# Optimization experiments

Hardware: AMD Instinct MI355X
Metric: run time of the kernel (lower is better)

Reference implementation:

```python
import jax, jax.numpy as jnp
import numpy as np

NEG_SLOPE = 0.1

def lrelu(x):
    return jnp.where(x >= 0, x, NEG_SLOPE * x)

def conv2d(x, w, b, padding=0, dilation=1):
    y = jax.lax.conv_general_dilated(
        x, w, window_strides=(1, 1),
        padding=[(padding, padding), (padding, padding)],
        rhs_dilation=(dilation, dilation),
        dimension_numbers=('NCHW', 'OIHW', 'NCHW'))
    return y + b[None, :, None, None]

def res_aspp(x, p):
    r1 = lrelu(conv2d(x, p['a1_w'], p['a1_b'], padding=1, dilation=1))
    r2 = lrelu(conv2d(x, p['a2_w'], p['a2_b'], padding=2, dilation=2))
    r3 = lrelu(conv2d(x, p['a3_w'], p['a3_b'], padding=4, dilation=4))
    r = conv2d(jnp.concatenate((r1, r2, r3), axis=1), p['ar_w'], p['ar_b'])
    return x + r

def deform_conv2d(x, offset, w, b):
    # x: [B,C,H,W], offset: [B,2*K,H,W] torchvision layout (y,x) per 3x3 tap
    B, C, H, W = x.shape
    KH = KW = 3
    K = KH * KW
    pad = 1
    off = offset.reshape(B, K, 2, H, W)
    ky, kx = jnp.meshgrid(jnp.arange(KH), jnp.arange(KW), indexing='ij')
    ky = ky.reshape(K).astype(x.dtype)
    kx = kx.reshape(K).astype(x.dtype)
    hh = jnp.arange(H, dtype=x.dtype)
    ww = jnp.arange(W, dtype=x.dtype)
    # sampling positions [B,K,H,W]
    py = off[:, :, 0] + (hh[None, None, :, None] - pad + ky[None, :, None, None])
    px = off[:, :, 1] + (ww[None, None, None, :] - pad + kx[None, :, None, None])
    y0 = jnp.floor(py)
    x0 = jnp.floor(px)
    wy = (py - y0)[:, None]  # [B,1,K,H,W]
    wx = (px - x0)[:, None]
    y0i = y0.astype(jnp.int32)
    x0i = x0.astype(jnp.int32)
    x_flat = x.reshape(B, C, H * W)

    def gather(iy, ix):
        valid = ((iy >= 0) & (iy < H) & (ix >= 0) & (ix < W)).astype(x.dtype)
        idx = jnp.clip(iy, 0, H - 1) * W + jnp.clip(ix, 0, W - 1)  # [B,K,H,W]
        v = jax.vmap(lambda xb, ib: xb[:, ib])(x_flat, idx.reshape(B, -1))
        return v.reshape(B, C, K, H, W) * valid[:, None]

    samp = (gather(y0i, x0i) * (1 - wy) * (1 - wx)
            + gather(y0i, x0i + 1) * (1 - wy) * wx
            + gather(y0i + 1, x0i) * wy * (1 - wx)
            + gather(y0i + 1, x0i + 1) * wy * wx)
    out = jnp.einsum('bckhw,ock->bohw', samp, w.reshape(w.shape[0], C, K))
    return out + b[None, :, None, None]

def setup_inputs() -> dict:
    key = jax.random.key(0)
    ks = jax.random.split(key, 16)
    B, C, H, W = 4, 64, 160, 160
    Cout = 64
    s = 0.05
    d = {
        'in_aux': jax.random.normal(ks[0], (B, C, H, W), jnp.float32),
        'in_ref': jax.random.normal(ks[1], (B, C, H, W), jnp.float32),
        'w01': jax.random.normal(ks[2], (Cout, 2 * C, 1, 1), jnp.float32) * s,
        'b01': jnp.zeros((Cout,), jnp.float32),
        'a1_w': jax.random.normal(ks[3], (Cout, Cout, 3, 3), jnp.float32) * s,
        'a1_b': jnp.zeros((Cout,), jnp.float32),
        'a2_w': jax.random.normal(ks[4], (Cout, Cout, 3, 3), jnp.float32) * s,
        'a2_b': jnp.zeros((Cout,), jnp.float32),
        'a3_w': jax.random.normal(ks[5], (Cout, Cout, 3, 3), jnp.float32) * s,
        'a3_b': jnp.zeros((Cout,), jnp.float32),
        'ar_w': jax.random.normal(ks[6], (Cout, 3 * Cout, 1, 1), jnp.float32) * s,
        'ar_b': jnp.zeros((Cout,), jnp.float32),
        'w02': jax.random.normal(ks[7], (18, Cout, 1, 1), jnp.float32) * s,
        'b02': jnp.zeros((18,), jnp.float32),
        'dw': jax.random.normal(ks[8], (Cout, C, 3, 3), jnp.float32) * s,
        'db': jnp.zeros((Cout,), jnp.float32),
    }
    return d

def reference(in_aux, in_ref, w01, b01, a1_w, a1_b, a2_w, a2_b, a3_w, a3_b,
              ar_w, ar_b, w02, b02, dw, db):
    cat_x = jnp.concatenate((in_aux, in_ref), axis=1)
    off_x = lrelu(conv2d(cat_x, w01, b01))
    p = {'a1_w': a1_w, 'a1_b': a1_b, 'a2_w': a2_w, 'a2_b': a2_b,
         'a3_w': a3_w, 'a3_b': a3_b, 'ar_w': ar_w, 'ar_b': ar_b}
    off_x = res_aspp(off_x, p)
    off_x = conv2d(off_x, w02, b02)
    return deform_conv2d(in_aux, off_x, dw, db)
```

## Files before the change

### kernel.cpp

```cpp
#include <hip/hip_runtime.h>
#include <math.h>

static constexpr int B = 4, H = 160, W = 160;
static constexpr int HW = H * W;
static constexpr int CHW = 64 * HW;
static constexpr int NELEM = B * CHW;

typedef short bf16x8 __attribute__((ext_vector_type(8)));
typedef float f32x4 __attribute__((ext_vector_type(4)));

__device__ __forceinline__ float lrelu(float v) { return v >= 0.f ? v : 0.1f * v; }

__device__ __forceinline__ unsigned short f2bf(float f) {
  unsigned u = __float_as_uint(f);
  return (unsigned short)((u + 0x7FFFu + ((u >> 16) & 1u)) >> 16);
}
__device__ __forceinline__ float bf2f(short u) {
  return __uint_as_float(((unsigned)(unsigned short)u) << 16);
}

__global__ __launch_bounds__(256) void k_transform(
    const float* __restrict__ w01, const float* __restrict__ dw,
    const float* __restrict__ arw, const float* __restrict__ a1w,
    const float* __restrict__ a2w, const float* __restrict__ a3w,
    float* __restrict__ wt01, unsigned short* __restrict__ wb_bf,
    unsigned short* __restrict__ wd_bf, unsigned short* __restrict__ arw_bf) {
  int i = blockIdx.x * 256 + threadIdx.x;
  if (i < 8192) {
    int ci = i >> 6, o = i & 63;
    wt01[i] = w01[o * 128 + ci];
  } else if (i < 118784) {
    int j = i - 8192;
    int ci = j & 63, co = (j >> 6) & 63;
    int kk = j >> 12;
    int dsel = kk / 9; kk -= dsel * 9;
    const float* src = dsel == 0 ? a1w : dsel == 1 ? a2w : a3w;
    wb_bf[j] = f2bf(src[(co * 64 + ci) * 9 + kk]);
  } else if (i < 155648) {
    int j = i - 118784;
    int ci = j & 63, co = (j >> 6) & 63, k = j >> 12;
    wd_bf[j] = f2bf(dw[(co * 64 + ci) * 9 + k]);
  } else if (i < 167936) {
    int j = i - 155648;
    arw_bf[j] = f2bf(arw[j]);
  }
}

__global__ __launch_bounds__(256) void k_conv1x1_in(
    const float* __restrict__ aux, const float* __restrict__ ref,
    const float* __restrict__ wt01, const float* __restrict__ b01,
    float* __restrict__ out, unsigned short* __restrict__ out_bf,
    unsigned short* __restrict__ x_bf) {
  __shared__ float s[128 * 64];
  int pos0 = blockIdx.x * 64;
  int b = pos0 / HW;
  int hw0 = pos0 - b * HW;
  int tid = threadIdx.x;
  for (int i = tid; i < 8192; i += 256) {
    int ci = i >> 6, p = i & 63;
    const float* src = (ci < 64) ? (aux + b * CHW + ci * HW)
                                 : (ref + b * CHW + (ci - 64) * HW);
    s[i] = src[hw0 + p];
  }
  __syncthreads();
  int p = tid & 63;
  int g = __builtin_amdgcn_readfirstlane(tid >> 6);
  const float* wp = wt01 + g * 16;
  float acc[16];
#pragma unroll
  for (int j = 0; j < 16; ++j) acc[j] = 0.f;
#pragma unroll 4
  for (int ci = 0; ci < 128; ++ci) {
    float sv = s[ci * 64 + p];
    const float* wrow = wp + ci * 64;
#pragma unroll
    for (int j = 0; j < 16; ++j) acc[j] += sv * wrow[j];
  }
  const float* bb = b01 + g * 16;
  int obase = (b * 64 + g * 16) * HW + hw0 + p;
  unsigned short tb[16];
#pragma unroll
  for (int j = 0; j < 16; ++j) {
    float v = lrelu(acc[j] + bb[j]);
    out[obase + j * HW] = v;
    tb[j] = f2bf(v);
  }
  unsigned short* dst = out_bf + ((size_t)(b * HW + hw0 + p)) * 64 + g * 16;
  *(uint4*)dst = *(const uint4*)&tb[0];
  *(uint4*)(dst + 8) = *(const uint4*)&tb[8];
  unsigned short xb[16];
#pragma unroll
  for (int j = 0; j < 16; ++j) xb[j] = f2bf(s[(g * 16 + j) * 64 + p]);
  unsigned short* xdst = x_bf + ((size_t)(b * HW + hw0 + p)) * 64 + g * 16;
  *(uint4*)xdst = *(const uint4*)&xb[0];
  *(uint4*)(xdst + 8) = *(const uint4*)&xb[8];
}

__global__ __launch_bounds__(256) void k_aspp3_mfma(
    const unsigned short* __restrict__ off0_bf,
    const unsigned short* __restrict__ wb_bf,
    const float* __restrict__ a1b, const float* __restrict__ a2b,
    const float* __restrict__ a3b, unsigned short* __restrict__ r_bf) {
  __shared__ unsigned short sin[576 * 40];
  int bx = blockIdx.x, by = blockIdx.y;
  int dsel = blockIdx.z >> 2, b = blockIdx.z & 3;
  int d = 1 << dsel;
  const float* bias = dsel == 0 ? a1b : dsel == 1 ? a2b : a3b;
  int tid = threadIdx.x;
  int lane = tid & 63, wid = tid >> 6;
  int m = lane & 15, q = lane >> 4;
  f32x4 acc[4][4] = {};
  const unsigned short* wbase = wb_bf + dsel * 9 * 4096;

  for (int ch = 0; ch < 2; ++ch) {
    __syncthreads();
    for (int i = tid; i < 2304; i += 256) {
      int pix = i >> 2, sub = i & 3;
      int py = pix / 24, px = pix - py * 24;
      int gy = by * 16 + py - 4, gx = bx * 16 + px - 4;
      uint4 v = make_uint4(0u, 0u, 0u, 0u);
      if (gy >= 0 && gy < H && gx >= 0 && gx < W)
        v = *(const uint4*)(off0_bf +
                            ((size_t)(b * HW + gy * W + gx)) * 64 + ch * 32 + sub * 8);
      *(uint4*)(sin + pix * 40 + sub * 8) = v;
    }
    __syncthreads();
#pragma unroll
    for (int k = 0; k < 9; ++k) {
      int ky = k / 3, kx = k - ky * 3;
      bf16x8 bfrag[4];
#pragma unroll
      for (int t = 0; t < 4; ++t)
        bfrag[t] = *(const bf16x8*)(wbase + ((k * 64 + t * 16 + m) * 64) + ch * 32 + q * 8);
      bf16x8 afrag[4];
#pragma unroll
      for (int mt = 0; mt < 4; ++mt) {
        int row = 4 + wid * 4 + mt + (ky - 1) * d;
        int col = 4 + m + (kx - 1) * d;
        afrag[mt] = *(const bf16x8*)(sin + (row * 24 + col) * 40 + q * 8);
      }
#pragma unroll
      for (int mt = 0; mt < 4; ++mt)
#pragma unroll
        for (int t = 0; t < 4; ++t)
          acc[mt][t] = __builtin_amdgcn_mfma_f32_16x16x32_bf16(
              afrag[mt], bfrag[t], acc[mt][t], 0, 0, 0);
    }
  }

  unsigned short* epb = sin;
  __syncthreads();
#pragma unroll
  for (int t = 0; t < 4; ++t) {
    float bi = bias[t * 16 + m];
#pragma unroll
    for (int mt = 0; mt < 4; ++mt) {
      int prow = wid * 4 + mt;
#pragma unroll
      for (int r = 0; r < 4; ++r) {
        int pix = prow * 16 + q * 4 + r;
        epb[pix * 72 + t * 16 + m] = f2bf(lrelu(acc[mt][t][r] + bi));
      }
    }
  }
  __syncthreads();
  {
    int pix = tid;
    int prow = pix >> 4, pcol = pix & 15;
    unsigned short* dst =
        r_bf + ((size_t)(b * HW + (by * 16 + prow) * W + bx * 16 + pcol)) * 192 +
        dsel * 64;
    const unsigned short* src = epb + pix * 72;
#pragma unroll
    for (int c = 0; c < 8; ++c)
      *(uint4*)(dst + c * 8) = *(const uint4*)(src + c * 8);
  }
}

__global__ __launch_bounds__(256) void k_merge_head_mfma(
    const unsigned short* __restrict__ r_bf, const float* __restrict__ off0,
    const unsigned short* __restrict__ arw_bf, const float* __restrict__ arb,
    const float* __restrict__ w02, const float* __restrict__ b02,
    float* __restrict__ offs) {
  __shared__ unsigned short sa[64 * 200];
  int pos0 = blockIdx.x * 64;
  int b = pos0 / HW;
  int hw0 = pos0 - b * HW;
  int tid = threadIdx.x;
  const unsigned short* gsrc = r_bf + (size_t)(b * HW + hw0) * 192;
  for (int i = tid; i < 1536; i += 256) {
    int pos = i / 24, c8 = i - pos * 24;
    *(uint4*)(sa + pos * 200 + c8 * 8) = *(const uint4*)(gsrc + i * 8);
  }
  __syncthreads();
  int lane = tid & 63, wid = tid >> 6;
  int m = lane & 15, q = lane >> 4;
  f32x4 acc[4] = {};
#pragma unroll
  for (int kc = 0; kc < 6; ++kc) {
    bf16x8 bfrag = *(const bf16x8*)(arw_bf + (wid * 16 + m) * 192 + kc * 32 + q * 8);
#pragma unroll
    for (int mt = 0; mt < 4; ++mt) {
      bf16x8 afrag = *(const bf16x8*)(sa + (mt * 16 + m) * 200 + kc * 32 + q * 8);
      acc[mt] = __builtin_amdgcn_mfma_f32_16x16x32_bf16(afrag, bfrag, acc[mt],
                                                        0, 0, 0);
    }
  }
  __syncthreads();
  float* ep = (float*)sa;
  int co = wid * 16 + m;
  float bi = arb[co];
  const float* resrow = off0 + (size_t)(b * 64 + co) * HW + hw0;
#pragma unroll
  for (int mt = 0; mt < 4; ++mt)
#pragma unroll
    for (int r = 0; r < 4; ++r) {
      int pos = mt * 16 + q * 4 + r;
      ep[pos * 65 + co] = acc[mt][r] + bi + resrow[pos];
    }
  __syncthreads();
  for (int i = tid; i < 1152; i += 256) {
    int t = i >> 6, p = i & 63;
    const float* w2 = w02 + t * 64;
    float o = b02[t];
#pragma unroll 8
    for (int c = 0; c < 64; ++c) o += ep[p * 65 + c] * w2[c];
    offs[(b * 18 + t) * HW + hw0 + p] = o;
  }
}

__global__ __launch_bounds__(256) void k_deform_mfma(
    const unsigned short* __restrict__ x_bf, const float* __restrict__ offs,
    const unsigned short* __restrict__ wd_bf, const float* __restrict__ db,
    float* __restrict__ out) {
  constexpr int SP = 72;
  __shared__ unsigned short sb[2][64 * SP];
  int blk = (blockIdx.x & 7) * 200 + (blockIdx.x >> 3);
  int pos0 = blk * 64;
  int b = pos0 / HW;
  int hw0 = pos0 - b * HW;
  int tid = threadIdx.x;
  int lane = tid & 63, wid = tid >> 6;
  int m = lane & 15, q = lane >> 4;
  int p = lane;
  int cg = wid;
  int hw = hw0 + p;
  int h = hw / W, wv = hw - h * W;
  const unsigned short* xb = x_bf + (size_t)b * HW * 64;
  const float* ob = offs + b * 18 * HW + hw;
  float offv[18];
#pragma unroll
  for (int j = 0; j < 18; ++j) offv[j] = ob[j * HW];
  f32x4 acc[4] = {};

#pragma unroll
  for (int k = 0; k < 9; ++k) {
    const int ky = k / 3, kx = k - ky * 3;
    float py = offv[2 * k] + (float)(h - 1 + ky);
    float px = offv[2 * k + 1] + (float)(wv - 1 + kx);
    float fy = floorf(py), fx = floorf(px);
    int iy0 = (int)fy, ix0 = (int)fx;
    float wy = py - fy, wx = px - fx;
    int iy1 = iy0 + 1, ix1 = ix0 + 1;
    float vy0 = (iy0 >= 0 && iy0 < H) ? 1.f : 0.f;
    float vy1 = (iy1 >= 0 && iy1 < H) ? 1.f : 0.f;
    float vx0 = (ix0 >= 0 && ix0 < W) ? 1.f : 0.f;
    float vx1 = (ix1 >= 0 && ix1 < W) ? 1.f : 0.f;
    int cy0 = min(max(iy0, 0), H - 1), cy1 = min(max(iy1, 0), H - 1);
    int cx0 = min(max(ix0, 0), W - 1), cx1 = min(max(ix1, 0), W - 1);
    float c00 = vy0 * vx0 * (1.f - wy) * (1.f - wx);
    float c01 = vy0 * vx1 * (1.f - wy) * wx;
    float c10 = vy1 * vx0 * wy * (1.f - wx);
    float c11 = vy1 * vx1 * wy * wx;
    const unsigned short* p00 = xb + (size_t)(cy0 * W + cx0) * 64 + cg * 16;
    const unsigned short* p01 = xb + (size_t)(cy0 * W + cx1) * 64 + cg * 16;
    const unsigned short* p10 = xb + (size_t)(cy1 * W + cx0) * 64 + cg * 16;
    const unsigned short* p11 = xb + (size_t)(cy1 * W + cx1) * 64 + cg * 16;
    unsigned short tb[16];
#pragma unroll
    for (int c2 = 0; c2 < 2; ++c2) {
      bf16x8 v00 = *(const bf16x8*)(p00 + c2 * 8);
      bf16x8 v01 = *(const bf16x8*)(p01 + c2 * 8);
      bf16x8 v10 = *(const bf16x8*)(p10 + c2 * 8);
      bf16x8 v11 = *(const bf16x8*)(p11 + c2 * 8);
#pragma unroll
      for (int j = 0; j < 8; ++j) {
        float sv = c00 * bf2f(v00[j]) + c01 * bf2f(v01[j]) +
                   c10 * bf2f(v10[j]) + c11 * bf2f(v11[j]);
        tb[c2 * 8 + j] = f2bf(sv);
      }
    }
    unsigned short* wr = &sb[k & 1][p * SP + cg * 16];
    *(uint4*)wr = *(const uint4*)&tb[0];
    *(uint4*)(wr + 8) = *(const uint4*)&tb[8];
    __syncthreads();
    const unsigned short* rb = &sb[k & 1][0];
#pragma unroll
    for (int kc = 0; kc < 2; ++kc) {
      bf16x8 bfrag =
          *(const bf16x8*)(wd_bf + (k * 64 + wid * 16 + m) * 64 + kc * 32 + q * 8);
#pragma unroll
      for (int mt = 0; mt < 4; ++mt) {
        bf16x8 afrag = *(const bf16x8*)(rb + (mt * 16 + m) * SP + kc * 32 + q * 8);
        acc[mt] = __builtin_amdgcn_mfma_f32_16x16x32_bf16(afrag, bfrag, acc[mt],
                                                          0, 0, 0);
      }
    }
  }
  int co = wid * 16 + m;
  float bias = db[co];
  size_t orow = (size_t)(b * 64 + co) * HW + hw0;
#pragma unroll
  for (int mt = 0; mt < 4; ++mt)
#pragma unroll
    for (int r = 0; r < 4; ++r)
      out[orow + mt * 16 + q * 4 + r] = acc[mt][r] + bias;
}

extern "C" void kernel_launch(void* const* d_in, const int* in_sizes, int n_in,
                              void* d_out, int out_size, void* d_ws, size_t ws_size,
                              hipStream_t stream) {
  const float* aux = (const float*)d_in[0];
  const float* ref = (const float*)d_in[1];
  const float* w01 = (const float*)d_in[2];
  const float* b01 = (const float*)d_in[3];
  const float* a1w = (const float*)d_in[4];
  const float* a1b = (const float*)d_in[5];
  const float* a2w = (const float*)d_in[6];
  const float* a2b = (const float*)d_in[7];
  const float* a3w = (const float*)d_in[8];
  const float* a3b = (const float*)d_in[9];
  const float* arw = (const float*)d_in[10];
  const float* arb = (const float*)d_in[11];
  const float* w02 = (const float*)d_in[12];
  const float* b02 = (const float*)d_in[13];
  const float* dw  = (const float*)d_in[14];
  const float* db  = (const float*)d_in[15];
  float* out = (float*)d_out;

  float* off0 = (float*)d_ws;
  float* offs = off0 + NELEM;
  float* wt01 = offs + B * 18 * HW;
  unsigned short* off0_bf = (unsigned short*)(wt01 + 8192);
  unsigned short* x_bf   = off0_bf + (size_t)NELEM;
  unsigned short* wb_bf  = x_bf + (size_t)NELEM;
  unsigned short* wd_bf  = wb_bf + 110592;
  unsigned short* arw_bf = wd_bf + 36864;
  unsigned short* r_bf   = arw_bf + 12288;

  k_transform<<<656, 256, 0, stream>>>(w01, dw, arw, a1w, a2w, a3w,
                                       wt01, wb_bf, wd_bf, arw_bf);
  k_conv1x1_in<<<B * HW / 64, 256, 0, stream>>>(aux, ref, wt01, b01, off0,
                                                off0_bf, x_bf);
  k_aspp3_mfma<<<dim3(10, 10, 12), 256, 0, stream>>>(
      off0_bf, wb_bf, a1b, a2b, a3b, r_bf);
  k_merge_head_mfma<<<B * HW / 64, 256, 0, stream>>>(
      r_bf, off0, arw_bf, arb, w02, b02, offs);
  k_deform_mfma<<<B * HW / 64, 256, 0, stream>>>(x_bf, offs, wd_bf, db, out);
}
```

Measured before the change: 333.3 us.

## Use MFMA for input 1x1 conv, direct global loads in ASPP, swizzled LDS

```diff
diff --git a/kernel.cpp b/kernel.cpp
--- a/kernel.cpp
+++ b/kernel.cpp
@@ -23,12 +23,11 @@
     const float* __restrict__ w01, const float* __restrict__ dw,
     const float* __restrict__ arw, const float* __restrict__ a1w,
     const float* __restrict__ a2w, const float* __restrict__ a3w,
-    float* __restrict__ wt01, unsigned short* __restrict__ wb_bf,
+    unsigned short* __restrict__ w01_bf, unsigned short* __restrict__ wb_bf,
     unsigned short* __restrict__ wd_bf, unsigned short* __restrict__ arw_bf) {
   int i = blockIdx.x * 256 + threadIdx.x;
   if (i < 8192) {
-    int ci = i >> 6, o = i & 63;
-    wt01[i] = w01[o * 128 + ci];
+    w01_bf[i] = f2bf(w01[i]);
   } else if (i < 118784) {
     int j = i - 8192;
     int ci = j & 63, co = (j >> 6) & 63;
@@ -46,54 +45,78 @@
   }
 }
 
-__global__ __launch_bounds__(256) void k_conv1x1_in(
+__global__ __launch_bounds__(256) void k_conv1x1_mfma(
     const float* __restrict__ aux, const float* __restrict__ ref,
-    const float* __restrict__ wt01, const float* __restrict__ b01,
-    float* __restrict__ out, unsigned short* __restrict__ out_bf,
+    const unsigned short* __restrict__ w01_bf, const float* __restrict__ b01,
+    float* __restrict__ off0p, unsigned short* __restrict__ off0_bf,
     unsigned short* __restrict__ x_bf) {
-  __shared__ float s[128 * 64];
+  __shared__ unsigned short sa[64 * 144];
   int pos0 = blockIdx.x * 64;
   int b = pos0 / HW;
   int hw0 = pos0 - b * HW;
   int tid = threadIdx.x;
-  for (int i = tid; i < 8192; i += 256) {
+#pragma unroll 4
+  for (int it = 0; it < 32; ++it) {
+    int i = it * 256 + tid;
     int ci = i >> 6, p = i & 63;
-    const float* src = (ci < 64) ? (aux + b * CHW + ci * HW)
-                                 : (ref + b * CHW + (ci - 64) * HW);
-    s[i] = src[hw0 + p];
-  }
-  __syncthreads();
-  int p = tid & 63;
-  int g = __builtin_amdgcn_readfirstlane(tid >> 6);
-  const float* wp = wt01 + g * 16;
-  float acc[16];
-#pragma unroll
-  for (int j = 0; j < 16; ++j) acc[j] = 0.f;
-#pragma unroll 4
-  for (int ci = 0; ci < 128; ++ci) {
-    float sv = s[ci * 64 + p];
-    const float* wrow = wp + ci * 64;
-#pragma unroll
-    for (int j = 0; j < 16; ++j) acc[j] += sv * wrow[j];
-  }
-  const float* bb = b01 + g * 16;
-  int obase = (b * 64 + g * 16) * HW + hw0 + p;
-  unsigned short tb[16];
-#pragma unroll
-  for (int j = 0; j < 16; ++j) {
-    float v = lrelu(acc[j] + bb[j]);
-    out[obase + j * HW] = v;
-    tb[j] = f2bf(v);
-  }
-  unsigned short* dst = out_bf + ((size_t)(b * HW + hw0 + p)) * 64 + g * 16;
-  *(uint4*)dst = *(const uint4*)&tb[0];
-  *(uint4*)(dst + 8) = *(const uint4*)&tb[8];
-  unsigned short xb[16];
-#pragma unroll
-  for (int j = 0; j < 16; ++j) xb[j] = f2bf(s[(g * 16 + j) * 64 + p]);
-  unsigned short* xdst = x_bf + ((size_t)(b * HW + hw0 + p)) * 64 + g * 16;
-  *(uint4*)xdst = *(const uint4*)&xb[0];
-  *(uint4*)(xdst + 8) = *(const uint4*)&xb[8];
+    float v = (ci < 64) ? aux[b * CHW + ci * HW + hw0 + p]
+                        : ref[b * CHW + (ci - 64) * HW + hw0 + p];
+    int key = (p >> 2) & 7;
+    sa[p * 144 + (((ci >> 3) ^ key) * 8) + (ci & 7)] = f2bf(v);
+  }
+  __syncthreads();
+  int lane = tid & 63, wid = tid >> 6;
+  int m = lane & 15, q = lane >> 4;
+  f32x4 acc[4] = {};
+#pragma unroll
+  for (int kc = 0; kc < 4; ++kc) {
+    bf16x8 bfrag = *(const bf16x8*)(w01_bf + (wid * 16 + m) * 128 + kc * 32 + q * 8);
+#pragma unroll
+    for (int mt = 0; mt < 4; ++mt) {
+      int row = mt * 16 + m;
+      int rkey = (row >> 2) & 7;
+      bf16x8 afrag = *(const bf16x8*)(sa + row * 144 + (((kc * 4 + q) ^ rkey) * 8));
+      acc[mt] = __builtin_amdgcn_mfma_f32_16x16x32_bf16(afrag, bfrag, acc[mt],
+                                                        0, 0, 0);
+    }
+  }
+#pragma unroll
+  for (int it = 0; it < 2; ++it) {
+    int u = it * 256 + tid;
+    int p = u >> 3, c = u & 7;
+    int key = (p >> 2) & 7;
+    uint4 v = *(const uint4*)(sa + p * 144 + ((c ^ key) * 8));
+    *(uint4*)(x_bf + ((size_t)(b * HW + hw0 + p)) * 64 + c * 8) = v;
+  }
+  float bi = b01[wid * 16 + m];
+  float vv[4][4];
+#pragma unroll
+  for (int mt = 0; mt < 4; ++mt)
+#pragma unroll
+    for (int r = 0; r < 4; ++r) {
+      float v = lrelu(acc[mt][r] + bi);
+      vv[mt][r] = v;
+      off0p[((size_t)(b * HW + hw0 + mt * 16 + q * 4 + r)) * 64 + wid * 16 + m] = v;
+    }
+  __syncthreads();
+#pragma unroll
+  for (int mt = 0; mt < 4; ++mt)
+#pragma unroll
+    for (int r = 0; r < 4; ++r) {
+      int pl = mt * 16 + q * 4 + r;
+      int chunk = wid * 2 + (m >> 3);
+      int key = (pl >> 2) & 7;
+      sa[pl * 80 + ((chunk ^ key) * 8) + (m & 7)] = f2bf(vv[mt][r]);
+    }
+  __syncthreads();
+#pragma unroll
+  for (int it = 0; it < 2; ++it) {
+    int u = it * 256 + tid;
+    int p = u >> 3, c = u & 7;
+    int key = (p >> 2) & 7;
+    uint4 v = *(const uint4*)(sa + p * 80 + ((c ^ key) * 8));
+    *(uint4*)(off0_bf + ((size_t)(b * HW + hw0 + p)) * 64 + c * 8) = v;
+  }
 }
 
 __global__ __launch_bounds__(256) void k_aspp3_mfma(
@@ -101,7 +124,7 @@
     const unsigned short* __restrict__ wb_bf,
     const float* __restrict__ a1b, const float* __restrict__ a2b,
     const float* __restrict__ a3b, unsigned short* __restrict__ r_bf) {
-  __shared__ unsigned short sin[576 * 40];
+  __shared__ unsigned short epb[256 * 80];
   int bx = blockIdx.x, by = blockIdx.y;
   int dsel = blockIdx.z >> 2, b = blockIdx.z & 3;
   int d = 1 << dsel;
@@ -111,33 +134,37 @@
   int m = lane & 15, q = lane >> 4;
   f32x4 acc[4][4] = {};
   const unsigned short* wbase = wb_bf + dsel * 9 * 4096;
-
-  for (int ch = 0; ch < 2; ++ch) {
-    __syncthreads();
-    for (int i = tid; i < 2304; i += 256) {
-      int pix = i >> 2, sub = i & 3;
-      int py = pix / 24, px = pix - py * 24;
-      int gy = by * 16 + py - 4, gx = bx * 16 + px - 4;
-      uint4 v = make_uint4(0u, 0u, 0u, 0u);
-      if (gy >= 0 && gy < H && gx >= 0 && gx < W)
-        v = *(const uint4*)(off0_bf +
-                            ((size_t)(b * HW + gy * W + gx)) * 64 + ch * 32 + sub * 8);
-      *(uint4*)(sin + pix * 40 + sub * 8) = v;
-    }
-    __syncthreads();
-#pragma unroll
-    for (int k = 0; k < 9; ++k) {
-      int ky = k / 3, kx = k - ky * 3;
+  const unsigned short* xoff = off0_bf + (size_t)b * HW * 64;
+  int ybase = by * 16 + wid * 4;
+  int xcol = bx * 16 + m;
+
+#pragma unroll 3
+  for (int k = 0; k < 9; ++k) {
+    int ky = k / 3, kx = k - ky * 3;
+    int gx = xcol + (kx - 1) * d;
+    bool vx = (unsigned)gx < (unsigned)W;
+    int gy[4];
+    bool vy[4];
+#pragma unroll
+    for (int mt = 0; mt < 4; ++mt) {
+      gy[mt] = ybase + mt + (ky - 1) * d;
+      vy[mt] = (unsigned)gy[mt] < (unsigned)H;
+    }
+#pragma unroll
+    for (int ch = 0; ch < 2; ++ch) {
       bf16x8 bfrag[4];
 #pragma unroll
       for (int t = 0; t < 4; ++t)
-        bfrag[t] = *(const bf16x8*)(wbase + ((k * 64 + t * 16 + m) * 64) + ch * 32 + q * 8);
+        bfrag[t] =
+            *(const bf16x8*)(wbase + (k * 64 + t * 16 + m) * 64 + ch * 32 + q * 8);
       bf16x8 afrag[4];
 #pragma unroll
       for (int mt = 0; mt < 4; ++mt) {
-        int row = 4 + wid * 4 + mt + (ky - 1) * d;
-        int col = 4 + m + (kx - 1) * d;
-        afrag[mt] = *(const bf16x8*)(sin + (row * 24 + col) * 40 + q * 8);
+        bf16x8 z = {0, 0, 0, 0, 0, 0, 0, 0};
+        afrag[mt] = z;
+        if (vy[mt] && vx)
+          afrag[mt] = *(const bf16x8*)(xoff + ((size_t)(gy[mt] * W + gx)) * 64 +
+                                       ch * 32 + q * 8);
       }
 #pragma unroll
       for (int mt = 0; mt < 4; ++mt)
@@ -148,8 +175,6 @@
     }
   }
 
-  unsigned short* epb = sin;
-  __syncthreads();
 #pragma unroll
   for (int t = 0; t < 4; ++t) {
     float bi = bias[t * 16 + m];
@@ -159,7 +184,10 @@
 #pragma unroll
       for (int r = 0; r < 4; ++r) {
         int pix = prow * 16 + q * 4 + r;
-        epb[pix * 72 + t * 16 + m] = f2bf(lrelu(acc[mt][t][r] + bi));
+        int chunk = t * 2 + (m >> 3);
+        int key = (pix >> 2) & 7;
+        epb[pix * 80 + ((chunk ^ key) * 8) + (m & 7)] =
+            f2bf(lrelu(acc[mt][t][r] + bi));
       }
     }
   }
@@ -167,18 +195,18 @@
   {
     int pix = tid;
     int prow = pix >> 4, pcol = pix & 15;
+    int key = (pix >> 2) & 7;
     unsigned short* dst =
         r_bf + ((size_t)(b * HW + (by * 16 + prow) * W + bx * 16 + pcol)) * 192 +
         dsel * 64;
-    const unsigned short* src = epb + pix * 72;
 #pragma unroll
     for (int c = 0; c < 8; ++c)
-      *(uint4*)(dst + c * 8) = *(const uint4*)(src + c * 8);
+      *(uint4*)(dst + c * 8) = *(const uint4*)(epb + pix * 80 + ((c ^ key) * 8));
   }
 }
 
 __global__ __launch_bounds__(256) void k_merge_head_mfma(
-    const unsigned short* __restrict__ r_bf, const float* __restrict__ off0,
+    const unsigned short* __restrict__ r_bf, const float* __restrict__ off0p,
     const unsigned short* __restrict__ arw_bf, const float* __restrict__ arb,
     const float* __restrict__ w02, const float* __restrict__ b02,
     float* __restrict__ offs) {
@@ -210,13 +238,13 @@
   float* ep = (float*)sa;
   int co = wid * 16 + m;
   float bi = arb[co];
-  const float* resrow = off0 + (size_t)(b * 64 + co) * HW + hw0;
+  const float* resb = off0p + (size_t)(b * HW + hw0) * 64;
 #pragma unroll
   for (int mt = 0; mt < 4; ++mt)
 #pragma unroll
     for (int r = 0; r < 4; ++r) {
       int pos = mt * 16 + q * 4 + r;
-      ep[pos * 65 + co] = acc[mt][r] + bi + resrow[pos];
+      ep[pos * 65 + co] = acc[mt][r] + bi + resb[pos * 64 + co];
     }
   __syncthreads();
   for (int i = tid; i < 1152; i += 256) {
@@ -338,10 +366,10 @@
   const float* db  = (const float*)d_in[15];
   float* out = (float*)d_out;
 
-  float* off0 = (float*)d_ws;
-  float* offs = off0 + NELEM;
-  float* wt01 = offs + B * 18 * HW;
-  unsigned short* off0_bf = (unsigned short*)(wt01 + 8192);
+  float* off0p = (float*)d_ws;
+  float* offs = off0p + NELEM;
+  unsigned short* w01_bf = (unsigned short*)(offs + B * 18 * HW);
+  unsigned short* off0_bf = w01_bf + 8192;
   unsigned short* x_bf   = off0_bf + (size_t)NELEM;
   unsigned short* wb_bf  = x_bf + (size_t)NELEM;
   unsigned short* wd_bf  = wb_bf + 110592;
@@ -349,12 +377,12 @@
   unsigned short* r_bf   = arw_bf + 12288;
 
   k_transform<<<656, 256, 0, stream>>>(w01, dw, arw, a1w, a2w, a3w,
-                                       wt01, wb_bf, wd_bf, arw_bf);
-  k_conv1x1_in<<<B * HW / 64, 256, 0, stream>>>(aux, ref, wt01, b01, off0,
-                                                off0_bf, x_bf);
+                                       w01_bf, wb_bf, wd_bf, arw_bf);
+  k_conv1x1_mfma<<<B * HW / 64, 256, 0, stream>>>(aux, ref, w01_bf, b01,
+                                                  off0p, off0_bf, x_bf);
   k_aspp3_mfma<<<dim3(10, 10, 12), 256, 0, stream>>>(
       off0_bf, wb_bf, a1b, a2b, a3b, r_bf);
   k_merge_head_mfma<<<B * HW / 64, 256, 0, stream>>>(
-      r_bf, off0, arw_bf, arb, w02, b02, offs);
+      r_bf, off0p, arw_bf, arb, w02, b02, offs);
   k_deform_mfma<<<B * HW / 64, 256, 0, stream>>>(x_bf, offs, wd_bf, db, out);
 }
```

New measurement: 333.4 us. About the same (+0.0%).
